# Performance work log

Hardware: AMD Instinct MI355X
Metric: run time of the kernel (lower is better)

Reference implementation:

```python
import jax, jax.numpy as jnp
import numpy as np

B, N, E = 2, 2048, 1024
HQ, HKV = 16, 4           # query heads, kv heads
G = HQ // HKV             # groups (== HKV by construction; required by source einsum)
D = E // HQ               # head_dim = 64
KV_E = D * HKV            # kv projection dim = 256
LN_EPS = 1e-5


def _layernorm(x, g, b):
    mu = jnp.mean(x, axis=-1, keepdims=True)
    var = jnp.mean(jnp.square(x - mu), axis=-1, keepdims=True)
    return (x - mu) * jax.lax.rsqrt(var + LN_EPS) * g + b


def setup_inputs() -> dict:
    key = jax.random.key(0)
    ks = jax.random.split(key, 5)
    s = 0.02
    return {
        "x": jax.random.normal(ks[0], (B, N, E), dtype=jnp.float32),
        "Wq": jax.random.normal(ks[1], (E, E), dtype=jnp.float32) * s,
        "Wk": jax.random.normal(ks[2], (E, KV_E), dtype=jnp.float32) * s,
        "Wv": jax.random.normal(ks[3], (E, KV_E), dtype=jnp.float32) * s,
        "Wout": jax.random.normal(ks[4], (E, E), dtype=jnp.float32) * s,
        "ln_g": jnp.ones((E,), dtype=jnp.float32),
        "ln_b": jnp.zeros((E,), dtype=jnp.float32),
    }


def reference(x, Wq, Wk, Wv, Wout, ln_g, ln_b):
    b, n, _ = x.shape
    # projections
    q = (x @ Wq).reshape(b, n, HQ, D).transpose(0, 2, 1, 3)   # b hq n d
    k = (x @ Wk).reshape(b, n, HKV, D).transpose(0, 2, 1, 3)  # b hkv s d
    v = (x @ Wv).reshape(b, n, HKV, D).transpose(0, 2, 1, 3)  # b hkv s d
    # split query heads: (h g) with h=HKV outer, g=G inner -> b hkv g n d
    q = q.reshape(b, HKV, G, n, D)
    scale = jnp.asarray(np.sqrt(D), dtype=x.dtype)
    scores = jnp.einsum('bhgnd,bhsd->bhgns', q, k) / scale    # b hkv g n s
    causal = jnp.tril(jnp.ones((n, n), dtype=bool))           # n s
    scores = jnp.where(causal[None, None, None, :, :], scores, jnp.asarray(-jnp.inf, x.dtype))
    attn = jax.nn.softmax(scores, axis=-1)                    # b i=hkv j=g n s
    # Faithful to source's mislabeled einsum: value head axis is indexed by the
    # GROUP index j (valid because G == HKV here).
    out = jnp.einsum('bijns,bjsd->bijnd', attn, v)            # b i j n d
    # rearrange 'b g h n d -> b n (h g) d' with g=i, h=j -> merged head order (j, i)
    out = out.transpose(0, 3, 2, 1, 4).reshape(b, n, HQ * D)  # b n E
    out = _layernorm(out, ln_g, ln_b) @ Wout
    # rearrange 'b g h n s -> b n s (h g)' then mean over n
    attn_w = attn.transpose(0, 3, 4, 2, 1).reshape(b, n, n, HQ).mean(axis=1)  # b s HQ
    return (out, attn_w)
```

## Files before the change

kernel.cpp:

```cpp
#include <hip/hip_runtime.h>

#define BB 2
#define NN 2048
#define EE 1024
#define HQH 16
#define DD 64
#define KVE 256
#define QKVW 1536

typedef short bf16x8 __attribute__((ext_vector_type(8)));
typedef short bf16x4 __attribute__((ext_vector_type(4)));
typedef float f32x4 __attribute__((ext_vector_type(4)));
typedef unsigned short u16;
typedef unsigned int u32;

#if __has_builtin(__builtin_amdgcn_exp2f)
#define EXP2(x) __builtin_amdgcn_exp2f(x)
#else
#define EXP2(x) exp2f(x)
#endif

#define QSCALE 0.18033688011112042f

__device__ __forceinline__ u16 f2bf(float f) {
    unsigned u = __float_as_uint(f);
    u += 0x7FFFu + ((u >> 16) & 1u);
    return (u16)(u >> 16);
}
__device__ __forceinline__ float bf2f(u16 h) {
    return __uint_as_float(((unsigned)h) << 16);
}
__device__ __forceinline__ u32 cvtpk(float a, float b) {
    u32 r;
    asm("v_cvt_pk_bf16_f32 %0, %1, %2" : "=v"(r) : "v"(a), "v"(b));
    return r;
}

#define GLOAD_LDS16(gp, lp) __builtin_amdgcn_global_load_lds( \
    (const __attribute__((address_space(1))) unsigned int*)(gp), \
    (__attribute__((address_space(3))) unsigned int*)(lp), 16, 0, 0)

__device__ __forceinline__ bf16x8 xpose8(bf16x8 v, int q) {
    union { bf16x8 v; u32 r[4]; } u_;
    u_.v = v;
    u32 r0 = u_.r[0], r1 = u_.r[1], r2 = u_.r[2], r3 = u_.r[3];
    u32 x, y, t0;
    x = (q & 4) ? r0 : r2;  y = (q & 4) ? r1 : r3;
    x = __shfl_xor(x, 4);   y = __shfl_xor(y, 4);
    if (q & 4) { r0 = x; r1 = y; } else { r2 = x; r3 = y; }
    x = (q & 2) ? r0 : r1;  y = (q & 2) ? r2 : r3;
    x = __shfl_xor(x, 2);   y = __shfl_xor(y, 2);
    if (q & 2) { r0 = x; r2 = y; } else { r1 = x; r3 = y; }
    t0 = __shfl_xor(r0, 1); r0 = (q & 1) ? ((t0 >> 16) | (r0 & 0xFFFF0000u)) : ((r0 & 0xFFFFu) | (t0 << 16));
    t0 = __shfl_xor(r1, 1); r1 = (q & 1) ? ((t0 >> 16) | (r1 & 0xFFFF0000u)) : ((r1 & 0xFFFFu) | (t0 << 16));
    t0 = __shfl_xor(r2, 1); r2 = (q & 1) ? ((t0 >> 16) | (r2 & 0xFFFF0000u)) : ((r2 & 0xFFFFu) | (t0 << 16));
    t0 = __shfl_xor(r3, 1); r3 = (q & 1) ? ((t0 >> 16) | (r3 & 0xFFFF0000u)) : ((r3 & 0xFFFFu) | (t0 << 16));
    u_.r[0] = r0; u_.r[1] = r1; u_.r[2] = r2; u_.r[3] = r3;
    return u_.v;
}

__global__ __launch_bounds__(256)
void conv_bf16(const float* __restrict__ in, u16* __restrict__ out) {
    int i = (blockIdx.x * 256 + threadIdx.x) * 8;
    float4 a = *(const float4*)&in[i];
    float4 b = *(const float4*)&in[i + 4];
    bf16x8 p;
    p[0] = f2bf(a.x); p[1] = f2bf(a.y); p[2] = f2bf(a.z); p[3] = f2bf(a.w);
    p[4] = f2bf(b.x); p[5] = f2bf(b.y); p[6] = f2bf(b.z); p[7] = f2bf(b.w);
    *(bf16x8*)&out[i] = p;
}

__global__ __launch_bounds__(256)
void transp_bf16(const float* __restrict__ W, u16* __restrict__ WT, int Nc) {
    __shared__ float tile[32][33];
    int k0 = blockIdx.x * 32, n0 = blockIdx.y * 32;
    int tx = threadIdx.x & 31, ty = threadIdx.x >> 5;
#pragma unroll
    for (int i = 0; i < 4; ++i)
        tile[ty + i * 8][tx] = W[(size_t)(k0 + ty + i * 8) * Nc + n0 + tx];
    __syncthreads();
#pragma unroll
    for (int i = 0; i < 4; ++i)
        WT[(size_t)(n0 + ty + i * 8) * EE + k0 + tx] = f2bf(tile[tx][ty + i * 8]);
}

__global__ __launch_bounds__(256)
void gemm_mfma(const u16* __restrict__ A, const u16* __restrict__ BT,
               void* __restrict__ C, int K, int ldc, int obf16,
               float qscale, int nq) {
    __shared__ __attribute__((aligned(16))) u16 sA[128 * 64];
    __shared__ __attribute__((aligned(16))) u16 sB[128 * 64];
    int t = threadIdx.x;
    int lane = t & 63, w = t >> 6;
    int wr = w >> 1, wc = w & 1;
    int l15 = lane & 15, lg = lane >> 4;
    int m0 = blockIdx.y * 128, n0 = blockIdx.x * 128;

    f32x4 acc[4][4];
#pragma unroll
    for (int mi = 0; mi < 4; ++mi)
#pragma unroll
        for (int ni = 0; ni < 4; ++ni) acc[mi][ni] = (f32x4){0.f, 0.f, 0.f, 0.f};

    int srow = lane >> 3;
    int schunk = (lane & 7) ^ srow;
    const u16* ga = A + (size_t)(m0 + w * 32 + srow) * K + schunk * 8;
    const u16* gb = BT + (size_t)(n0 + w * 32 + srow) * K + schunk * 8;
    char* lA = (char*)sA + w * 4096;
    char* lB = (char*)sB + w * 4096;

    for (int k0 = 0; k0 < K; k0 += 64) {
#pragma unroll
        for (int i = 0; i < 4; ++i) {
            GLOAD_LDS16(ga + (size_t)i * 8 * K + k0, lA + i * 1024);
            GLOAD_LDS16(gb + (size_t)i * 8 * K + k0, lB + i * 1024);
        }
        __syncthreads();
#pragma unroll
        for (int ks = 0; ks < 2; ++ks) {
            bf16x8 af[4], bfr[4];
#pragma unroll
            for (int mi = 0; mi < 4; ++mi) {
                int row = wr * 64 + mi * 16 + l15;
                af[mi] = *(const bf16x8*)((char*)sA +
                    ((row * 128 + lg * 16 + ks * 64) ^ ((row & 7) << 4)));
            }
#pragma unroll
            for (int ni = 0; ni < 4; ++ni) {
                int row = wc * 64 + ni * 16 + l15;
                bfr[ni] = *(const bf16x8*)((char*)sB +
                    ((row * 128 + lg * 16 + ks * 64) ^ ((row & 7) << 4)));
            }
#pragma unroll
            for (int mi = 0; mi < 4; ++mi)
#pragma unroll
                for (int ni = 0; ni < 4; ++ni)
                    acc[mi][ni] = __builtin_amdgcn_mfma_f32_16x16x32_bf16(
                        af[mi], bfr[ni], acc[mi][ni], 0, 0, 0);
        }
        __syncthreads();
    }

#pragma unroll
    for (int mi = 0; mi < 4; ++mi) {
        int rbase = m0 + wr * 64 + mi * 16 + lg * 4;
#pragma unroll
        for (int ni = 0; ni < 4; ++ni) {
            int col = n0 + wc * 64 + ni * 16 + l15;
            float sc = (col < nq) ? qscale : 1.0f;
            if (obf16) {
                u16* Cb = (u16*)C;
#pragma unroll
                for (int r = 0; r < 4; ++r)
                    Cb[(size_t)(rbase + r) * ldc + col] = f2bf(acc[mi][ni][r] * sc);
            } else {
                float* Cf = (float*)C;
#pragma unroll
                for (int r = 0; r < 4; ++r)
                    Cf[(size_t)(rbase + r) * ldc + col] = acc[mi][ni][r] * sc;
            }
        }
    }
}

__global__ __launch_bounds__(256)
void flash_attn(const u16* __restrict__ QKV, u16* __restrict__ AOb,
                float* __restrict__ lbuf) {
    __shared__ __attribute__((aligned(16))) u16 sV[2][64 * 64];

    int blk = blockIdx.x;
    int ntile = 15 - (blk & 15);
    int bh = blk >> 4;
    int hq = bh & 15;
    int b = bh >> 4;
    int ih = hq >> 2, jh = hq & 3;
    int hm = jh * 4 + ih;
    int n0 = ntile * 128;
    int t = threadIdx.x;
    int lane = t & 63, w = t >> 6;
    int l15 = lane & 15, lg = lane >> 4;
    int q8 = t & 7;

    const u16* Kg = QKV + (size_t)b * NN * QKVW + EE + ih * DD;
    const u16* Vg = QKV + (size_t)b * NN * QKVW + EE + KVE + jh * DD;

    bf16x8 qf[2][2];
#pragma unroll
    for (int tt = 0; tt < 2; ++tt)
#pragma unroll
        for (int h = 0; h < 2; ++h)
            qf[tt][h] = *(const bf16x8*)(QKV +
                (size_t)(b * NN + n0 + w * 32 + tt * 16 + l15) * QKVW + hq * DD + lg * 8 + h * 32);

    f32x4 o[2][4];
    float lrow[2] = {0.f, 0.f};
#pragma unroll
    for (int tt = 0; tt < 2; ++tt)
#pragma unroll
        for (int i = 0; i < 4; ++i) o[tt][i] = (f32x4){0.f, 0.f, 0.f, 0.f};

    int nt = (n0 + 128) >> 6;
    bf16x8 vr[2];
#pragma unroll
    for (int it = 0; it < 2; ++it) {
        int lin = t + it * 256;
        vr[it] = *(const bf16x8*)(Vg + (size_t)((lin >> 6) * 8 + q8) * QKVW + ((lin >> 3) & 7) * 8);
    }
#pragma unroll
    for (int it = 0; it < 2; ++it) {
        int lin = t + it * 256;
        int d = ((lin >> 3) & 7) * 8 + q8;
        int sbase = (lin >> 6) * 8;
        bf16x8 vt = xpose8(vr[it], q8);
        *(bf16x8*)((char*)sV[0] + ((d * 128 + sbase * 2) ^ (q8 << 4))) = vt;
    }

    for (int ti = 0; ti < nt; ++ti) {
        int s0 = ti << 6;
        if (ti + 1 < nt) {
#pragma unroll
            for (int it = 0; it < 2; ++it) {
                int lin = t + it * 256;
                vr[it] = *(const bf16x8*)(Vg +
                    (size_t)(s0 + 64 + (lin >> 6) * 8 + q8) * QKVW + ((lin >> 3) & 7) * 8);
            }
        }
        __syncthreads();
        const char* vb = (const char*)sV[ti & 1];

        bf16x8 k0[4], k1[4];
#pragma unroll
        for (int sub = 0; sub < 4; ++sub) {
            const u16* kp = Kg + (size_t)(s0 + sub * 16 + l15) * QKVW + lg * 8;
            k0[sub] = *(const bf16x8*)kp;
            k1[sub] = *(const bf16x8*)(kp + 32);
        }
        f32x4 sf[2][4];
        __builtin_amdgcn_s_setprio(1);
#pragma unroll
        for (int sub = 0; sub < 4; ++sub)
#pragma unroll
            for (int tt = 0; tt < 2; ++tt) {
                f32x4 z = {0.f, 0.f, 0.f, 0.f};
                z = __builtin_amdgcn_mfma_f32_16x16x32_bf16(k0[sub], qf[tt][0], z, 0, 0, 0);
                sf[tt][sub] = __builtin_amdgcn_mfma_f32_16x16x32_bf16(k1[sub], qf[tt][1], z, 0, 0, 0);
            }
        __builtin_amdgcn_s_setprio(0);

        bf16x8 vf[4][2];
#pragma unroll
        for (int sd = 0; sd < 4; ++sd) {
            int d = sd * 16 + l15;
            int swz = (d & 7) << 4;
#pragma unroll
            for (int f = 0; f < 2; ++f) {
                int aA = (d * 128 + (f * 32 + lg * 4) * 2) ^ swz;
                int aB = (d * 128 + (f * 32 + 16 + lg * 4) * 2) ^ swz;
                bf16x4 lo = *(const bf16x4*)(vb + aA);
                bf16x4 hi = *(const bf16x4*)(vb + aB);
                bf16x8 vv;
                vv[0] = lo[0]; vv[1] = lo[1]; vv[2] = lo[2]; vv[3] = lo[3];
                vv[4] = hi[0]; vv[5] = hi[1]; vv[6] = hi[2]; vv[7] = hi[3];
                vf[sd][f] = vv;
            }
        }

#pragma unroll
        for (int tt = 0; tt < 2; ++tt) {
            int ng_min = n0 + w * 32 + tt * 16;
            int ng = ng_min + l15;
            float rs = 0.f;
            if (s0 + 63 > ng_min) {
#pragma unroll
                for (int sub = 0; sub < 4; ++sub)
#pragma unroll
                    for (int r = 0; r < 4; ++r) {
                        int sg = s0 + sub * 16 + lg * 4 + r;
                        float p = (sg <= ng) ? EXP2(sf[tt][sub][r]) : 0.f;
                        sf[tt][sub][r] = p;
                        rs += p;
                    }
            } else {
#pragma unroll
                for (int sub = 0; sub < 4; ++sub)
#pragma unroll
                    for (int r = 0; r < 4; ++r) {
                        float p = EXP2(sf[tt][sub][r]);
                        sf[tt][sub][r] = p;
                        rs += p;
                    }
            }
            rs += __shfl_xor(rs, 16);
            rs += __shfl_xor(rs, 32);
            lrow[tt] += rs;

            union { u32 r[4]; bf16x8 v; } pa0, pa1;
            pa0.r[0] = cvtpk(sf[tt][0][0], sf[tt][0][1]);
            pa0.r[1] = cvtpk(sf[tt][0][2], sf[tt][0][3]);
            pa0.r[2] = cvtpk(sf[tt][1][0], sf[tt][1][1]);
            pa0.r[3] = cvtpk(sf[tt][1][2], sf[tt][1][3]);
            pa1.r[0] = cvtpk(sf[tt][2][0], sf[tt][2][1]);
            pa1.r[1] = cvtpk(sf[tt][2][2], sf[tt][2][3]);
            pa1.r[2] = cvtpk(sf[tt][3][0], sf[tt][3][1]);
            pa1.r[3] = cvtpk(sf[tt][3][2], sf[tt][3][3]);
            __builtin_amdgcn_s_setprio(1);
#pragma unroll
            for (int sd = 0; sd < 4; ++sd) {
                o[tt][sd] = __builtin_amdgcn_mfma_f32_16x16x32_bf16(pa0.v, vf[sd][0], o[tt][sd], 0, 0, 0);
                o[tt][sd] = __builtin_amdgcn_mfma_f32_16x16x32_bf16(pa1.v, vf[sd][1], o[tt][sd], 0, 0, 0);
            }
            __builtin_amdgcn_s_setprio(0);
        }

        if (ti + 1 < nt) {
#pragma unroll
            for (int it = 0; it < 2; ++it) {
                int lin = t + it * 256;
                int d = ((lin >> 3) & 7) * 8 + q8;
                int sbase = (lin >> 6) * 8;
                bf16x8 vt = xpose8(vr[it], q8);
                *(bf16x8*)((char*)sV[(ti + 1) & 1] + ((d * 128 + sbase * 2) ^ (q8 << 4))) = vt;
            }
        }
    }

#pragma unroll
    for (int tt = 0; tt < 2; ++tt) {
        float linv = 1.f / lrow[tt];
        if (lg == 0) {
            int n = n0 + w * 32 + tt * 16 + l15;
            lbuf[(size_t)bh * NN + n] = linv;
        }
        float i0 = __shfl(linv, lg * 4 + 0);
        float i1 = __shfl(linv, lg * 4 + 1);
        float i2 = __shfl(linv, lg * 4 + 2);
        float i3 = __shfl(linv, lg * 4 + 3);
#pragma unroll
        for (int sd = 0; sd < 4; ++sd) {
            int nb = n0 + w * 32 + tt * 16 + lg * 4;
            size_t base = (size_t)(b * NN + nb) * EE + hm * DD + sd * 16 + l15;
            AOb[base]          = f2bf(o[tt][sd][0] * i0);
            AOb[base + EE]     = f2bf(o[tt][sd][1] * i1);
            AOb[base + 2 * EE] = f2bf(o[tt][sd][2] * i2);
            AOb[base + 3 * EE] = f2bf(o[tt][sd][3] * i3);
        }
    }
}

__global__ __launch_bounds__(256)
void colsum_mfma(const u16* __restrict__ QKV, const float* __restrict__ lbuf,
                 float* __restrict__ AW) {
    int blk = blockIdx.x;
    int stile = blk & 15;
    int bh = blk >> 4;
    int hq = bh & 15;
    int b = bh >> 4;
    int ih = hq >> 2, jh = hq & 3;
    int hm = jh * 4 + ih;
    int t = threadIdx.x;
    int lane = t & 63, w = t >> 6;
    int l15 = lane & 15, lg = lane >> 4;
    int sb = stile * 128 + w * 32;

    bf16x8 kf[2][2];
#pragma unroll
    for (int st = 0; st < 2; ++st)
#pragma unroll
        for (int h = 0; h < 2; ++h)
            kf[st][h] = *(const bf16x8*)(QKV +
                (size_t)(b * NN + sb + st * 16 + l15) * QKVW + EE + ih * DD + lg * 8 + h * 32);

    float acc[2][4] = {};
    int nstart = stile * 128;

    for (int nn0 = nstart; nn0 < NN; nn0 += 64) {
        bf16x8 qc[4][2];
        float lv[4];
#pragma unroll
        for (int c = 0; c < 4; ++c) {
            const u16* qp = QKV + (size_t)(b * NN + nn0 + c * 16 + l15) * QKVW + hq * DD + lg * 8;
            qc[c][0] = *(const bf16x8*)qp;
            qc[c][1] = *(const bf16x8*)(qp + 32);
            lv[c] = lbuf[(size_t)bh * NN + nn0 + c * 16 + l15];
        }
#pragma unroll
        for (int c = 0; c < 4; ++c) {
            int n = nn0 + c * 16 + l15;
#pragma unroll
            for (int st = 0; st < 2; ++st) {
                f32x4 z = {0.f, 0.f, 0.f, 0.f};
                z = __builtin_amdgcn_mfma_f32_16x16x32_bf16(kf[st][0], qc[c][0], z, 0, 0, 0);
                z = __builtin_amdgcn_mfma_f32_16x16x32_bf16(kf[st][1], qc[c][1], z, 0, 0, 0);
#pragma unroll
                for (int r = 0; r < 4; ++r) {
                    int s = sb + st * 16 + lg * 4 + r;
                    float val = EXP2(z[r]) * lv[c];
                    acc[st][r] += (n >= s) ? val : 0.f;
                }
            }
        }
    }
#pragma unroll
    for (int st = 0; st < 2; ++st)
#pragma unroll
        for (int r = 0; r < 4; ++r) {
            float a = acc[st][r];
            a += __shfl_xor(a, 1);
            a += __shfl_xor(a, 2);
            a += __shfl_xor(a, 4);
            a += __shfl_xor(a, 8);
            if (l15 == 0) {
                int s = sb + st * 16 + lg * 4 + r;
                AW[((size_t)b * NN + s) * HQH + hm] = a * (1.0f / NN);
            }
        }
}

__global__ __launch_bounds__(256)
void layernorm_bf16(u16* __restrict__ X, const float* __restrict__ g,
                    const float* __restrict__ bt) {
    __shared__ float red[256];
    int row = blockIdx.x;
    int t = threadIdx.x;
    u16* xp = X + (size_t)row * EE;
    ushort4 v = *(ushort4*)&xp[t * 4];
    float x0 = bf2f(v.x), x1 = bf2f(v.y), x2 = bf2f(v.z), x3 = bf2f(v.w);
    red[t] = x0 + x1 + x2 + x3;
    __syncthreads();
    for (int off = 128; off > 0; off >>= 1) {
        if (t < off) red[t] += red[t + off];
        __syncthreads();
    }
    float mu = red[0] * (1.f / EE);
    __syncthreads();
    float d0 = x0 - mu, d1 = x1 - mu, d2 = x2 - mu, d3 = x3 - mu;
    red[t] = d0 * d0 + d1 * d1 + d2 * d2 + d3 * d3;
    __syncthreads();
    for (int off = 128; off > 0; off >>= 1) {
        if (t < off) red[t] += red[t + off];
        __syncthreads();
    }
    float rstd = rsqrtf(red[0] * (1.f / EE) + 1e-5f);
    float4 gg = *(const float4*)&g[t * 4];
    float4 bb = *(const float4*)&bt[t * 4];
    ushort4 o;
    o.x = f2bf(d0 * rstd * gg.x + bb.x);
    o.y = f2bf(d1 * rstd * gg.y + bb.y);
    o.z = f2bf(d2 * rstd * gg.z + bb.z);
    o.w = f2bf(d3 * rstd * gg.w + bb.w);
    *(ushort4*)&xp[t * 4] = o;
}

extern "C" void kernel_launch(void* const* d_in, const int* in_sizes, int n_in,
                              void* d_out, int out_size, void* d_ws, size_t ws_size,
                              hipStream_t stream) {
    const float* x    = (const float*)d_in[0];
    const float* Wq   = (const float*)d_in[1];
    const float* Wk   = (const float*)d_in[2];
    const float* Wv   = (const float*)d_in[3];
    const float* Wout = (const float*)d_in[4];
    const float* lng  = (const float*)d_in[5];
    const float* lnb  = (const float*)d_in[6];

    float* out = (float*)d_out;
    float* aw  = out + (size_t)BB * NN * EE;

    u16* Xb    = (u16*)d_ws;
    u16* QKVb  = Xb + (size_t)BB * NN * EE;
    u16* WqkvT = QKVb + (size_t)BB * NN * QKVW;
    u16* WoutT = WqkvT + (size_t)QKVW * EE;
    u16* AOb   = WoutT + (size_t)EE * EE;
    float* lb  = (float*)(AOb + (size_t)BB * NN * EE);

    dim3 blk(256);

    conv_bf16<<<BB * NN * EE / 2048, blk, 0, stream>>>(x, Xb);
    transp_bf16<<<dim3(32, 32), blk, 0, stream>>>(Wq, WqkvT, EE);
    transp_bf16<<<dim3(32, 8), blk, 0, stream>>>(Wk, WqkvT + (size_t)EE * EE, KVE);
    transp_bf16<<<dim3(32, 8), blk, 0, stream>>>(Wv, WqkvT + (size_t)(EE + KVE) * EE, KVE);
    transp_bf16<<<dim3(32, 32), blk, 0, stream>>>(Wout, WoutT, EE);

    gemm_mfma<<<dim3(QKVW / 128, BB * NN / 128), blk, 0, stream>>>(
        Xb, WqkvT, QKVb, EE, QKVW, 1, QSCALE, EE);

    int ablocks = BB * HQH * 16;
    flash_attn<<<ablocks, blk, 0, stream>>>(QKVb, AOb, lb);
    colsum_mfma<<<ablocks, blk, 0, stream>>>(QKVb, lb, aw);

    layernorm_bf16<<<BB * NN, blk, 0, stream>>>(AOb, lng, lnb);

    gemm_mfma<<<dim3(EE / 128, BB * NN / 128), blk, 0, stream>>>(
        AOb, WoutT, out, EE, EE, 0, 1.0f, 0);
}
```

Measured before the change: 291.0 us.

## Prefetch K tiles and Q chunks with register double buffering, rebalance block order

In flash_attn, the next K tile is now loaded into registers during the current iteration. This uses a ping-pong pair of register arrays and unrolls the loop by two, so global K latency overlaps the MFMA work. The V fragment LDS reads are also moved ahead of the QK MFMAs. colsum_mfma gets the same double buffering for Q chunks and l values. Both kernels remap block indices so heavy and light causal tiles interleave across the grid, which should balance load. The cost is higher register pressure, which may lower occupancy.

```diff
diff --git a/kernel.cpp b/kernel.cpp
--- a/kernel.cpp
+++ b/kernel.cpp
@@ -169,8 +169,10 @@
     __shared__ __attribute__((aligned(16))) u16 sV[2][64 * 64];
 
     int blk = blockIdx.x;
-    int ntile = 15 - (blk & 15);
-    int bh = blk >> 4;
+    int hi = blk >> 8;
+    int mid = (blk >> 5) & 7;
+    int bh = blk & 31;
+    int ntile = hi ? mid : (15 - mid);
     int hq = bh & 15;
     int b = bh >> 4;
     int ih = hq >> 2, jh = hq & 3;
@@ -200,6 +202,7 @@
         for (int i = 0; i < 4; ++i) o[tt][i] = (f32x4){0.f, 0.f, 0.f, 0.f};
 
     int nt = (n0 + 128) >> 6;
+
     bf16x8 vr[2];
 #pragma unroll
     for (int it = 0; it < 2; ++it) {
@@ -215,7 +218,16 @@
         *(bf16x8*)((char*)sV[0] + ((d * 128 + sbase * 2) ^ (q8 << 4))) = vt;
     }
 
-    for (int ti = 0; ti < nt; ++ti) {
+    bf16x8 ka0[4], ka1[4], kb0[4], kb1[4];
+#pragma unroll
+    for (int sub = 0; sub < 4; ++sub) {
+        const u16* kp = Kg + (size_t)(sub * 16 + l15) * QKVW + lg * 8;
+        ka0[sub] = *(const bf16x8*)kp;
+        ka1[sub] = *(const bf16x8*)(kp + 32);
+    }
+
+    auto body = [&](int ti, bf16x8 (&kc0)[4], bf16x8 (&kc1)[4],
+                    bf16x8 (&kn0)[4], bf16x8 (&kn1)[4]) {
         int s0 = ti << 6;
         if (ti + 1 < nt) {
 #pragma unroll
@@ -228,42 +240,44 @@
         __syncthreads();
         const char* vb = (const char*)sV[ti & 1];
 
-        bf16x8 k0[4], k1[4];
-#pragma unroll
-        for (int sub = 0; sub < 4; ++sub) {
-            const u16* kp = Kg + (size_t)(s0 + sub * 16 + l15) * QKVW + lg * 8;
-            k0[sub] = *(const bf16x8*)kp;
-            k1[sub] = *(const bf16x8*)(kp + 32);
-        }
-        f32x4 sf[2][4];
-        __builtin_amdgcn_s_setprio(1);
-#pragma unroll
-        for (int sub = 0; sub < 4; ++sub)
-#pragma unroll
-            for (int tt = 0; tt < 2; ++tt) {
-                f32x4 z = {0.f, 0.f, 0.f, 0.f};
-                z = __builtin_amdgcn_mfma_f32_16x16x32_bf16(k0[sub], qf[tt][0], z, 0, 0, 0);
-                sf[tt][sub] = __builtin_amdgcn_mfma_f32_16x16x32_bf16(k1[sub], qf[tt][1], z, 0, 0, 0);
-            }
-        __builtin_amdgcn_s_setprio(0);
-
-        bf16x8 vf[4][2];
+        if (ti + 1 < nt) {
+#pragma unroll
+            for (int sub = 0; sub < 4; ++sub) {
+                const u16* kp = Kg + (size_t)(s0 + 64 + sub * 16 + l15) * QKVW + lg * 8;
+                kn0[sub] = *(const bf16x8*)kp;
+                kn1[sub] = *(const bf16x8*)(kp + 32);
+            }
+        }
+
+        bf16x8 vf0[4], vf1[4];
 #pragma unroll
         for (int sd = 0; sd < 4; ++sd) {
             int d = sd * 16 + l15;
             int swz = (d & 7) << 4;
-#pragma unroll
-            for (int f = 0; f < 2; ++f) {
-                int aA = (d * 128 + (f * 32 + lg * 4) * 2) ^ swz;
-                int aB = (d * 128 + (f * 32 + 16 + lg * 4) * 2) ^ swz;
-                bf16x4 lo = *(const bf16x4*)(vb + aA);
-                bf16x4 hi = *(const bf16x4*)(vb + aB);
-                bf16x8 vv;
-                vv[0] = lo[0]; vv[1] = lo[1]; vv[2] = lo[2]; vv[3] = lo[3];
-                vv[4] = hi[0]; vv[5] = hi[1]; vv[6] = hi[2]; vv[7] = hi[3];
-                vf[sd][f] = vv;
-            }
-        }
+            bf16x4 f0lo = *(const bf16x4*)(vb + ((d * 128 + (lg * 4) * 2) ^ swz));
+            bf16x4 f0hi = *(const bf16x4*)(vb + ((d * 128 + (16 + lg * 4) * 2) ^ swz));
+            bf16x4 f1lo = *(const bf16x4*)(vb + ((d * 128 + (32 + lg * 4) * 2) ^ swz));
+            bf16x4 f1hi = *(const bf16x4*)(vb + ((d * 128 + (48 + lg * 4) * 2) ^ swz));
+            bf16x8 v0, v1;
+            v0[0] = f0lo[0]; v0[1] = f0lo[1]; v0[2] = f0lo[2]; v0[3] = f0lo[3];
+            v0[4] = f0hi[0]; v0[5] = f0hi[1]; v0[6] = f0hi[2]; v0[7] = f0hi[3];
+            v1[0] = f1lo[0]; v1[1] = f1lo[1]; v1[2] = f1lo[2]; v1[3] = f1lo[3];
+            v1[4] = f1hi[0]; v1[5] = f1hi[1]; v1[6] = f1hi[2]; v1[7] = f1hi[3];
+            vf0[sd] = v0;
+            vf1[sd] = v1;
+        }
+
+        f32x4 sf[2][4];
+        __builtin_amdgcn_s_setprio(1);
+#pragma unroll
+        for (int sub = 0; sub < 4; ++sub)
+#pragma unroll
+            for (int tt = 0; tt < 2; ++tt) {
+                f32x4 z = {0.f, 0.f, 0.f, 0.f};
+                z = __builtin_amdgcn_mfma_f32_16x16x32_bf16(kc0[sub], qf[tt][0], z, 0, 0, 0);
+                sf[tt][sub] = __builtin_amdgcn_mfma_f32_16x16x32_bf16(kc1[sub], qf[tt][1], z, 0, 0, 0);
+            }
+        __builtin_amdgcn_s_setprio(0);
 
 #pragma unroll
         for (int tt = 0; tt < 2; ++tt) {
@@ -306,8 +320,8 @@
             __builtin_amdgcn_s_setprio(1);
 #pragma unroll
             for (int sd = 0; sd < 4; ++sd) {
-                o[tt][sd] = __builtin_amdgcn_mfma_f32_16x16x32_bf16(pa0.v, vf[sd][0], o[tt][sd], 0, 0, 0);
-                o[tt][sd] = __builtin_amdgcn_mfma_f32_16x16x32_bf16(pa1.v, vf[sd][1], o[tt][sd], 0, 0, 0);
+                o[tt][sd] = __builtin_amdgcn_mfma_f32_16x16x32_bf16(pa0.v, vf0[sd], o[tt][sd], 0, 0, 0);
+                o[tt][sd] = __builtin_amdgcn_mfma_f32_16x16x32_bf16(pa1.v, vf1[sd], o[tt][sd], 0, 0, 0);
             }
             __builtin_amdgcn_s_setprio(0);
         }
@@ -322,6 +336,11 @@
                 *(bf16x8*)((char*)sV[(ti + 1) & 1] + ((d * 128 + sbase * 2) ^ (q8 << 4))) = vt;
             }
         }
+    };
+
+    for (int ti = 0; ti < nt; ti += 2) {
+        body(ti, ka0, ka1, kb0, kb1);
+        body(ti + 1, kb0, kb1, ka0, ka1);
     }
 
 #pragma unroll
@@ -351,8 +370,10 @@
 void colsum_mfma(const u16* __restrict__ QKV, const float* __restrict__ lbuf,
                  float* __restrict__ AW) {
     int blk = blockIdx.x;
-    int stile = blk & 15;
-    int bh = blk >> 4;
+    int hi = blk >> 8;
+    int mid = (blk >> 5) & 7;
+    int bh = blk & 31;
+    int stile = hi ? (15 - mid) : mid;
     int hq = bh & 15;
     int b = bh >> 4;
     int ih = hq >> 2, jh = hq & 3;
@@ -373,9 +394,10 @@
     float acc[2][4] = {};
     int nstart = stile * 128;
 
-    for (int nn0 = nstart; nn0 < NN; nn0 += 64) {
-        bf16x8 qc[4][2];
-        float lv[4];
+    bf16x8 qA[4][2], qB[4][2];
+    float lA[4], lB[4];
+
+    auto loadchunk = [&](int nn0, bf16x8 (&qc)[4][2], float (&lv)[4]) {
 #pragma unroll
         for (int c = 0; c < 4; ++c) {
             const u16* qp = QKV + (size_t)(b * NN + nn0 + c * 16 + l15) * QKVW + hq * DD + lg * 8;
@@ -383,6 +405,8 @@
             qc[c][1] = *(const bf16x8*)(qp + 32);
             lv[c] = lbuf[(size_t)bh * NN + nn0 + c * 16 + l15];
         }
+    };
+    auto compute = [&](int nn0, bf16x8 (&qc)[4][2], float (&lv)[4]) {
 #pragma unroll
         for (int c = 0; c < 4; ++c) {
             int n = nn0 + c * 16 + l15;
@@ -398,6 +422,16 @@
                     acc[st][r] += (n >= s) ? val : 0.f;
                 }
             }
+        }
+    };
+
+    loadchunk(nstart, qA, lA);
+    for (int nn0 = nstart; nn0 < NN; nn0 += 128) {
+        if (nn0 + 64 < NN) loadchunk(nn0 + 64, qB, lB);
+        compute(nn0, qA, lA);
+        if (nn0 + 64 < NN) {
+            if (nn0 + 128 < NN) loadchunk(nn0 + 128, qA, lA);
+            compute(nn0 + 64, qB, lB);
         }
     }
 #pragma unroll
```

New measurement: 278.6 us. 1.04x faster.
